# Kernel optimization log

Measured on AMD Instinct MI355X. Metric: run time of the kernel, lower is better.

The kernel has to match this reference:

```python
import jax, jax.numpy as jnp
import numpy as np

B, D, E, H = 8192, 2048, 8, 128

def setup_inputs() -> dict:
    key = jax.random.key(0)
    ks = jax.random.split(key, 9)
    s_d = 1.0 / np.sqrt(D)
    s_h = 1.0 / np.sqrt(H)
    return {
        "x": jax.random.normal(ks[0], (B, D), dtype=jnp.float32),
        "gate_w": jax.random.normal(ks[1], (D, E), dtype=jnp.float32) * s_d,
        "gate_b": jnp.zeros((E,), dtype=jnp.float32),
        "W1": jax.random.normal(ks[2], (E, D, H), dtype=jnp.float32) * s_d,
        "b1": jnp.zeros((E, H), dtype=jnp.float32),
        "W2": jax.random.normal(ks[3], (E, H, H), dtype=jnp.float32) * s_h,
        "b2": jnp.zeros((E, H), dtype=jnp.float32),
        "W3": jax.random.normal(ks[4], (E, H, D), dtype=jnp.float32) * s_h,
        "b3": jnp.zeros((E, D), dtype=jnp.float32),
    }

def reference(x, gate_w, gate_b, W1, b1, W2, b2, W3, b3):
    # Adaptive gate: softmax over experts
    gates = jax.nn.softmax(x @ gate_w + gate_b, axis=1)          # [B, E]
    # All experts as one batched (grouped) GEMM over the expert axis.
    h1 = jax.nn.silu(jnp.einsum('bd,edh->ebh', x, W1) + b1[:, None, :])   # [E, B, H]
    h2 = jax.nn.silu(jnp.einsum('ebh,ehk->ebk', h1, W2) + b2[:, None, :]) # [E, B, H]
    y = jnp.einsum('ebh,ehd->ebd', h2, W3) + b3[:, None, :]               # [E, B, D]
    # Gate-weighted sum over experts (fused reduction, no [B,E,D] stack kept)
    out = jnp.einsum('be,ebd->bd', gates, y)                     # [B, D]
    return out
```

## Files before the change

### kernel.cpp

```cpp
#include <hip/hip_runtime.h>


typedef __attribute__((ext_vector_type(8))) short short8;
typedef __attribute__((ext_vector_type(4))) float f32x4;

#define B_SZ 8192
#define D_SZ 2048
#define E_SZ 8
#define H_SZ 128
#define TILE_ELEMS 8192

__device__ __forceinline__ short f2bf(float f) {
  unsigned u = __builtin_bit_cast(unsigned, f);
  unsigned r = (u + 0x7fffu + ((u >> 16) & 1u)) >> 16;
  return (short)r;
}

__device__ __forceinline__ float silu_f(float v) {
  return v / (1.f + __expf(-v));
}

__device__ __forceinline__ void gload_lds16(const void* g, void* l) {
  __builtin_amdgcn_global_load_lds(
      (const __attribute__((address_space(1))) void*)g,
      (__attribute__((address_space(3))) void*)l,
      16, 0, 0);
}

template<int NKT>
__device__ __forceinline__ void gemm_core(const short* __restrict__ Ab,
                                          const short* __restrict__ Bb,
                                          short* lds, f32x4 acc[4][4])
{
  const int tid  = threadIdx.x;
  const int lane = tid & 63;
  const int wid  = tid >> 6;
  const int wr = wid >> 1, wc = wid & 1;
  const int lm = lane & 15, lk = lane >> 4;
  const int wbase = tid & ~63;
  short* As = lds;
  short* Bs = lds + 2 * TILE_ELEMS;

  #pragma unroll
  for (int q = 0; q < 4; ++q) {
    gload_lds16(Ab + (q*256 + tid)*8, As + (q*256 + wbase)*8);
    gload_lds16(Bb + (q*256 + tid)*8, Bs + (q*256 + wbase)*8);
  }
  __syncthreads();

  for (int kt = 0; kt < NKT; ++kt) {
    const int cur = kt & 1;
    if (kt + 1 < NKT) {
      const short* ga = Ab + (size_t)(kt+1)*TILE_ELEMS;
      const short* gb = Bb + (size_t)(kt+1)*TILE_ELEMS;
      short* la = As + (cur^1)*TILE_ELEMS;
      short* lb = Bs + (cur^1)*TILE_ELEMS;
      #pragma unroll
      for (int q = 0; q < 4; ++q) {
        gload_lds16(ga + (q*256 + tid)*8, la + (q*256 + wbase)*8);
        gload_lds16(gb + (q*256 + tid)*8, lb + (q*256 + wbase)*8);
      }
    }
    const short* Ac = As + cur*TILE_ELEMS;
    const short* Bc = Bs + cur*TILE_ELEMS;
    #pragma unroll
    for (int ks = 0; ks < 2; ++ks) {
      short8 av[4], bv[4];
      #pragma unroll
      for (int f = 0; f < 4; ++f)
        av[f] = *(const short8*)(Ac + (ks*4 + lk)*1024 + (wr*64 + f*16 + lm)*8);
      #pragma unroll
      for (int f = 0; f < 4; ++f)
        bv[f] = *(const short8*)(Bc + (ks*4 + lk)*1024 + (wc*64 + f*16 + lm)*8);
      #pragma unroll
      for (int i = 0; i < 4; ++i)
        #pragma unroll
        for (int j = 0; j < 4; ++j)
          acc[i][j] = __builtin_amdgcn_mfma_f32_16x16x32_bf16(av[i], bv[j], acc[i][j], 0, 0, 0);
    }
    __syncthreads();
  }
}

__global__ __launch_bounds__(256)
void k_convert(const float* __restrict__ x,  const float* __restrict__ W1,
               const float* __restrict__ W2, const float* __restrict__ W3,
               short* __restrict__ xf, short* __restrict__ w1f,
               short* __restrict__ w2f, short* __restrict__ w3f)
{
  const int gi = blockIdx.x * 256 + threadIdx.x;
  if (gi < 2097152) {
    const int t = gi >> 10, r = gi & 1023;
    const int bt = t >> 5, kt = t & 31;
    const int kg = r >> 7, p = r & 127;
    const float* src = x + (size_t)(bt*128 + p)*2048 + kt*64 + kg*8;
    const float4 v0 = *(const float4*)src;
    const float4 v1 = *(const float4*)(src + 4);
    short8 o;
    o[0]=f2bf(v0.x); o[1]=f2bf(v0.y); o[2]=f2bf(v0.z); o[3]=f2bf(v0.w);
    o[4]=f2bf(v1.x); o[5]=f2bf(v1.y); o[6]=f2bf(v1.z); o[7]=f2bf(v1.w);
    *(short8*)(xf + (size_t)gi*8) = o;
  } else if (gi < 2097152 + 262144) {
    const int g = gi - 2097152;
    const int t = g >> 10, r = g & 1023;
    const int e = t >> 5, kt = t & 31;
    const int kg = r >> 7, p = r & 127;
    const int k0 = kt*64 + kg*8;
    short8 o;
    #pragma unroll
    for (int j = 0; j < 8; ++j)
      o[j] = f2bf(W1[(size_t)e*262144 + (size_t)(k0 + j)*128 + p]);
    *(short8*)(w1f + (size_t)g*8) = o;
  } else if (gi < 2097152 + 262144 + 16384) {
    const int g = gi - (2097152 + 262144);
    const int t = g >> 10, r = g & 1023;
    const int e = t >> 1, kt = t & 1;
    const int kg = r >> 7, p = r & 127;
    const int k0 = kt*64 + kg*8;
    short8 o;
    #pragma unroll
    for (int j = 0; j < 8; ++j)
      o[j] = f2bf(W2[(size_t)e*16384 + (size_t)(k0 + j)*128 + p]);
    *(short8*)(w2f + (size_t)g*8) = o;
  } else if (gi < 2637824) {
    const int g = gi - 2375680;
    const int t = g >> 10, r = g & 1023;
    const int nt = t >> 4, kt = t & 15;
    const int kg = r >> 7, p = r & 127;
    const int k0 = kt*64 + kg*8;
    short8 o;
    #pragma unroll
    for (int j = 0; j < 8; ++j) {
      const int k = k0 + j;
      o[j] = f2bf(W3[(size_t)(k >> 7)*262144 + (size_t)(k & 127)*2048 + nt*128 + p]);
    }
    *(short8*)(w3f + (size_t)g*8) = o;
  }
}

__global__ __launch_bounds__(256)
void k_gate(const float* __restrict__ x, const float* __restrict__ gw,
            const float* __restrict__ gb, float* __restrict__ gates)
{
  const int wid = threadIdx.x >> 6, lane = threadIdx.x & 63;
  const int row = blockIdx.x * 4 + wid;
  const float* xr = x + (size_t)row * 2048;
  float acc[8] = {0.f,0.f,0.f,0.f,0.f,0.f,0.f,0.f};
  for (int it = 0; it < 32; ++it) {
    const int k = it*64 + lane;
    const float xv = xr[k];
    const float4 g0 = *(const float4*)(gw + (size_t)k*8);
    const float4 g1 = *(const float4*)(gw + (size_t)k*8 + 4);
    acc[0] += xv*g0.x; acc[1] += xv*g0.y; acc[2] += xv*g0.z; acc[3] += xv*g0.w;
    acc[4] += xv*g1.x; acc[5] += xv*g1.y; acc[6] += xv*g1.z; acc[7] += xv*g1.w;
  }
  #pragma unroll
  for (int e = 0; e < 8; ++e) {
    #pragma unroll
    for (int d = 1; d < 64; d <<= 1)
      acc[e] += __shfl_xor(acc[e], d, 64);
  }
  if (lane == 0) {
    float lg[8], mx = -1e30f;
    #pragma unroll
    for (int e = 0; e < 8; ++e) { lg[e] = acc[e] + gb[e]; mx = fmaxf(mx, lg[e]); }
    float s = 0.f;
    #pragma unroll
    for (int e = 0; e < 8; ++e) { lg[e] = __expf(lg[e] - mx); s += lg[e]; }
    const float inv = 1.f / s;
    #pragma unroll
    for (int e = 0; e < 8; ++e) gates[(size_t)row*8 + e] = lg[e] * inv;
  }
}

__global__ __launch_bounds__(256, 2)
void k_gemm1(const short* __restrict__ xf, const short* __restrict__ w1f,
             const float* __restrict__ b1, short* __restrict__ h1f)
{
  __shared__ short lds[4 * TILE_ELEMS];
  const int bt = blockIdx.x, e = blockIdx.y;
  f32x4 acc[4][4] = {};
  gemm_core<32>(xf + (size_t)bt*32*TILE_ELEMS, w1f + (size_t)e*32*TILE_ELEMS, lds, acc);

  const int tid = threadIdx.x, lane = tid & 63, wid = tid >> 6;
  const int wr = wid >> 1, wc = wid & 1, lm = lane & 15;
  float bv[4];
  #pragma unroll
  for (int fn = 0; fn < 4; ++fn) bv[fn] = b1[e*H_SZ + wc*64 + fn*16 + lm];
  #pragma unroll
  for (int fm = 0; fm < 4; ++fm)
  #pragma unroll
  for (int i = 0; i < 4; ++i) {
    const int m = wr*64 + fm*16 + (lane>>4)*4 + i;
    #pragma unroll
    for (int fn = 0; fn < 4; ++fn) {
      const int n = wc*64 + fn*16 + lm;
      float v = silu_f(acc[fm][fn][i] + bv[fn]);
      lds[(n>>6)*TILE_ELEMS + ((n>>3)&7)*1024 + m*8 + (n&7)] = f2bf(v);
    }
  }
  __syncthreads();
  short* gout = h1f + (size_t)e*1048576 + (size_t)bt*16384;
  #pragma unroll
  for (int q = 0; q < 8; ++q) {
    const int li = q*256 + tid;
    *(short8*)(gout + li*8) = *(const short8*)(lds + li*8);
  }
}

__global__ __launch_bounds__(256, 2)
void k_gemm2(const short* __restrict__ h1f, const short* __restrict__ w2f,
             const float* __restrict__ b2, const float* __restrict__ gates,
             short* __restrict__ h2gf)
{
  __shared__ short lds[4 * TILE_ELEMS];
  const int bt = blockIdx.x, e = blockIdx.y;
  f32x4 acc[4][4] = {};
  gemm_core<2>(h1f + (size_t)e*1048576 + (size_t)bt*16384,
               w2f + (size_t)e*2*TILE_ELEMS, lds, acc);

  const int tid = threadIdx.x, lane = tid & 63, wid = tid >> 6;
  const int wr = wid >> 1, wc = wid & 1, lm = lane & 15;
  float bv[4];
  #pragma unroll
  for (int fn = 0; fn < 4; ++fn) bv[fn] = b2[e*H_SZ + wc*64 + fn*16 + lm];
  #pragma unroll
  for (int fm = 0; fm < 4; ++fm)
  #pragma unroll
  for (int i = 0; i < 4; ++i) {
    const int m = wr*64 + fm*16 + (lane>>4)*4 + i;
    const float g = gates[(size_t)(bt*128 + m)*8 + e];
    #pragma unroll
    for (int fn = 0; fn < 4; ++fn) {
      const int n = wc*64 + fn*16 + lm;
      float v = silu_f(acc[fm][fn][i] + bv[fn]) * g;
      lds[(n>>6)*TILE_ELEMS + ((n>>3)&7)*1024 + m*8 + (n&7)] = f2bf(v);
    }
  }
  __syncthreads();
  short* gout = h2gf + (size_t)bt*16384*8 + (size_t)e*16384;
  #pragma unroll
  for (int q = 0; q < 8; ++q) {
    const int li = q*256 + tid;
    *(short8*)(gout + li*8) = *(const short8*)(lds + li*8);
  }
}

__global__ __launch_bounds__(256, 2)
void k_gemm3(const short* __restrict__ h2gf, const short* __restrict__ w3f,
             const float* __restrict__ b3, const float* __restrict__ gates,
             float* __restrict__ out)
{
  __shared__ short lds[4 * TILE_ELEMS];
  const int bt = blockIdx.x, nt = blockIdx.y;
  f32x4 acc[4][4] = {};
  gemm_core<16>(h2gf + (size_t)bt*16*TILE_ELEMS, w3f + (size_t)nt*16*TILE_ELEMS, lds, acc);

  const int tid = threadIdx.x, lane = tid & 63, wid = tid >> 6;
  const int wr = wid >> 1, wc = wid & 1, lm = lane & 15;
  float b3c[4][8];
  #pragma unroll
  for (int fn = 0; fn < 4; ++fn) {
    const int n = nt*128 + wc*64 + fn*16 + lm;
    #pragma unroll
    for (int e = 0; e < 8; ++e) b3c[fn][e] = b3[(size_t)e*D_SZ + n];
  }
  #pragma unroll
  for (int fm = 0; fm < 4; ++fm)
  #pragma unroll
  for (int i = 0; i < 4; ++i) {
    const int m = bt*128 + wr*64 + fm*16 + (lane>>4)*4 + i;
    const float4 ga = *(const float4*)(gates + (size_t)m*8);
    const float4 gbv = *(const float4*)(gates + (size_t)m*8 + 4);
    #pragma unroll
    for (int fn = 0; fn < 4; ++fn) {
      const int n = nt*128 + wc*64 + fn*16 + lm;
      const float bias = ga.x*b3c[fn][0] + ga.y*b3c[fn][1] + ga.z*b3c[fn][2] + ga.w*b3c[fn][3]
                       + gbv.x*b3c[fn][4] + gbv.y*b3c[fn][5] + gbv.z*b3c[fn][6] + gbv.w*b3c[fn][7];
      out[(size_t)m*D_SZ + n] = acc[fm][fn][i] + bias;
    }
  }
}

extern "C" void kernel_launch(void* const* d_in, const int* in_sizes, int n_in,
                              void* d_out, int out_size, void* d_ws, size_t ws_size,
                              hipStream_t stream)
{
  (void)in_sizes; (void)n_in; (void)out_size; (void)ws_size;
  const float* x  = (const float*)d_in[0];
  const float* gw = (const float*)d_in[1];
  const float* gb = (const float*)d_in[2];
  const float* W1 = (const float*)d_in[3];
  const float* b1 = (const float*)d_in[4];
  const float* W2 = (const float*)d_in[5];
  const float* b2 = (const float*)d_in[6];
  const float* W3 = (const float*)d_in[7];
  const float* b3 = (const float*)d_in[8];
  float* out = (float*)d_out;

  char* ws = (char*)d_ws;
  short* xf    = (short*)ws;  ws += (size_t)B_SZ*D_SZ*2;
  short* w1f   = (short*)ws;  ws += (size_t)E_SZ*D_SZ*H_SZ*2;
  short* w2f   = (short*)ws;  ws += (size_t)E_SZ*H_SZ*H_SZ*2;
  short* w3f   = (short*)ws;  ws += (size_t)E_SZ*H_SZ*D_SZ*2;
  float* gates = (float*)ws;  ws += (size_t)B_SZ*E_SZ*4;
  short* h1f   = (short*)ws;  ws += (size_t)E_SZ*B_SZ*H_SZ*2;
  short* h2gf  = (short*)ws;  ws += (size_t)B_SZ*E_SZ*H_SZ*2;

  k_convert<<<dim3(10304), dim3(256), 0, stream>>>(x, W1, W2, W3, xf, w1f, w2f, w3f);
  k_gate   <<<dim3(2048),  dim3(256), 0, stream>>>(x, gw, gb, gates);
  k_gemm1  <<<dim3(64, 8), dim3(256), 0, stream>>>(xf, w1f, b1, h1f);
  k_gemm2  <<<dim3(64, 8), dim3(256), 0, stream>>>(h1f, w2f, b2, gates, h2gf);
  k_gemm3  <<<dim3(64, 16), dim3(256), 0, stream>>>(h2gf, w3f, b3, gates, out);
}
```

Baseline: 151.2 us.

## Use 8-wave 256x128 tiles with double-buffered half-K pipelined GEMM core

Adds a new GEMM core for gemm1 and gemm3 that uses 512-thread blocks computing 256x128 output tiles, with double-buffered LDS staging split into K halves. Global-to-LDS loads for upcoming stages overlap MFMA work, using explicit vmcnt waits, barriers and raised MFMA priority. The larger tile improves B-operand reuse and halves the grid. The risks are higher LDS usage and lower occupancy, and the hand-placed waits and barriers are fragile to get right.

```diff
diff --git a/kernel.cpp b/kernel.cpp
--- a/kernel.cpp
+++ b/kernel.cpp
@@ -10,6 +10,11 @@
 #define H_SZ 128
 #define TILE_ELEMS 8192
 
+#define VMCNT(n) asm volatile("s_waitcnt vmcnt(" #n ")" ::: "memory")
+#define LGKM0()  asm volatile("s_waitcnt lgkmcnt(0)" ::: "memory")
+#define SB0()    __builtin_amdgcn_sched_barrier(0)
+#define BAR()    __builtin_amdgcn_s_barrier()
+
 __device__ __forceinline__ short f2bf(float f) {
   unsigned u = __builtin_bit_cast(unsigned, f);
   unsigned r = (u + 0x7fffu + ((u >> 16) & 1u)) >> 16;
@@ -25,6 +30,94 @@
       (const __attribute__((address_space(1))) void*)g,
       (__attribute__((address_space(3))) void*)l,
       16, 0, 0);
+}
+
+template<int NKT>
+__device__ __forceinline__ void core8(const short* __restrict__ Ab,
+                                      const short* __restrict__ Bb,
+                                      short* lds, f32x4 acc[4][4])
+{
+  const int tid  = threadIdx.x;
+  const int lane = tid & 63;
+  const int wid  = tid >> 6;
+  const int wm = wid >> 1, wn = wid & 1;
+  const int rt = wm >> 1, rh = wm & 1;
+  const int lm = lane & 15, lk = lane >> 4;
+  const int wlds = (tid & ~63) * 8;
+
+  auto STAGE = [&](int b, int tau, int kh) {
+    const int boff = b * 24576;
+    gload_lds16(Ab + (size_t)(0*NKT + tau)*8192 + kh*4096 + tid*8,
+                lds + boff + 0*8192 + kh*4096 + wlds);
+    gload_lds16(Ab + (size_t)(1*NKT + tau)*8192 + kh*4096 + tid*8,
+                lds + boff + 1*8192 + kh*4096 + wlds);
+    gload_lds16(Bb + (size_t)tau*8192 + kh*4096 + tid*8,
+                lds + boff + 16384 + kh*4096 + wlds);
+  };
+  auto READ_A = [&](int ks, int cur, short8 av[4]) {
+    const short* Ac = lds + cur*24576 + rt*8192 + (ks*4+lk)*1024 + (rh*64 + lm)*8;
+    #pragma unroll
+    for (int f = 0; f < 4; ++f) av[f] = *(const short8*)(Ac + f*128);
+  };
+  auto READ_B = [&](int ks, int cur, short8 bv[4]) {
+    const short* Bc = lds + cur*24576 + 16384 + (ks*4+lk)*1024 + (wn*64 + lm)*8;
+    #pragma unroll
+    for (int f = 0; f < 4; ++f) bv[f] = *(const short8*)(Bc + f*128);
+  };
+  auto MFMA16 = [&](short8 av[4], short8 bv[4]) {
+    __builtin_amdgcn_s_setprio(1);
+    #pragma unroll
+    for (int i = 0; i < 4; ++i)
+      #pragma unroll
+      for (int j = 0; j < 4; ++j)
+        acc[i][j] = __builtin_amdgcn_mfma_f32_16x16x32_bf16(av[i], bv[j], acc[i][j], 0, 0, 0);
+    __builtin_amdgcn_s_setprio(0);
+  };
+
+  STAGE(0, 0, 0);
+  STAGE(0, 0, 1);
+  STAGE(1, 1, 0);
+  VMCNT(6); BAR();
+
+  for (int t = 0; t < NKT - 2; ++t) {
+    const int cur = t & 1;
+    short8 av[4], bv[4];
+    READ_A(0, cur, av); READ_B(0, cur, bv);
+    STAGE(cur ^ 1, t + 1, 1);
+    BAR(); LGKM0(); SB0();
+    MFMA16(av, bv);
+    SB0(); VMCNT(6); BAR();
+    READ_A(1, cur, av); READ_B(1, cur, bv);
+    STAGE(cur, t + 2, 0);
+    BAR(); LGKM0(); SB0();
+    MFMA16(av, bv);
+    SB0(); VMCNT(6); BAR();
+  }
+  {
+    const int cur = (NKT - 2) & 1;
+    short8 av[4], bv[4];
+    READ_A(0, cur, av); READ_B(0, cur, bv);
+    STAGE(cur ^ 1, NKT - 1, 1);
+    BAR(); LGKM0(); SB0();
+    MFMA16(av, bv);
+    SB0(); VMCNT(6); BAR();
+    READ_A(1, cur, av); READ_B(1, cur, bv);
+    BAR(); LGKM0(); SB0();
+    MFMA16(av, bv);
+    SB0(); VMCNT(3); BAR();
+  }
+  {
+    const int cur = (NKT - 1) & 1;
+    short8 av[4], bv[4];
+    READ_A(0, cur, av); READ_B(0, cur, bv);
+    BAR(); LGKM0(); SB0();
+    MFMA16(av, bv);
+    SB0(); VMCNT(0); BAR();
+    READ_A(1, cur, av); READ_B(1, cur, bv);
+    BAR(); LGKM0(); SB0();
+    MFMA16(av, bv);
+    SB0();
+  }
 }
 
 template<int NKT>
@@ -173,38 +266,41 @@
   }
 }
 
-__global__ __launch_bounds__(256, 2)
+__global__ __launch_bounds__(512, 2)
 void k_gemm1(const short* __restrict__ xf, const short* __restrict__ w1f,
              const float* __restrict__ b1, short* __restrict__ h1f)
 {
-  __shared__ short lds[4 * TILE_ELEMS];
+  __shared__ short lds[49152];
   const int bt = blockIdx.x, e = blockIdx.y;
   f32x4 acc[4][4] = {};
-  gemm_core<32>(xf + (size_t)bt*32*TILE_ELEMS, w1f + (size_t)e*32*TILE_ELEMS, lds, acc);
-
+  core8<32>(xf + (size_t)(bt*2)*32*8192, w1f + (size_t)e*32*8192, lds, acc);
+
+  __syncthreads();
   const int tid = threadIdx.x, lane = tid & 63, wid = tid >> 6;
-  const int wr = wid >> 1, wc = wid & 1, lm = lane & 15;
+  const int wm = wid >> 1, wn = wid & 1, lm = lane & 15, lr = lane >> 4;
   float bv[4];
   #pragma unroll
-  for (int fn = 0; fn < 4; ++fn) bv[fn] = b1[e*H_SZ + wc*64 + fn*16 + lm];
+  for (int fn = 0; fn < 4; ++fn) bv[fn] = b1[e*H_SZ + wn*64 + fn*16 + lm];
   #pragma unroll
   for (int fm = 0; fm < 4; ++fm)
   #pragma unroll
   for (int i = 0; i < 4; ++i) {
-    const int m = wr*64 + fm*16 + (lane>>4)*4 + i;
+    const int m = wm*64 + fm*16 + lr*4 + i;
     #pragma unroll
     for (int fn = 0; fn < 4; ++fn) {
-      const int n = wc*64 + fn*16 + lm;
+      const int n = wn*64 + fn*16 + lm;
       float v = silu_f(acc[fm][fn][i] + bv[fn]);
-      lds[(n>>6)*TILE_ELEMS + ((n>>3)&7)*1024 + m*8 + (n&7)] = f2bf(v);
+      lds[(m>>7)*16384 + (n>>6)*8192 + ((n>>3)&7)*1024 + (m&127)*8 + (n&7)] = f2bf(v);
     }
   }
   __syncthreads();
-  short* gout = h1f + (size_t)e*1048576 + (size_t)bt*16384;
   #pragma unroll
   for (int q = 0; q < 8; ++q) {
-    const int li = q*256 + tid;
-    *(short8*)(gout + li*8) = *(const short8*)(lds + li*8);
+    const int li = q*4096 + tid*8;
+    const int ti = li >> 13, o = li & 8191;
+    const int rt_o = ti >> 1, kt_o = ti & 1;
+    short* dst = h1f + ((size_t)(e*64 + bt*2 + rt_o)*2 + kt_o)*8192 + o;
+    *(short8*)dst = *(const short8*)(lds + li);
   }
 }
 
@@ -246,22 +342,22 @@
   }
 }
 
-__global__ __launch_bounds__(256, 2)
+__global__ __launch_bounds__(512, 2)
 void k_gemm3(const short* __restrict__ h2gf, const short* __restrict__ w3f,
              const float* __restrict__ b3, const float* __restrict__ gates,
              float* __restrict__ out)
 {
-  __shared__ short lds[4 * TILE_ELEMS];
+  __shared__ short lds[49152];
   const int bt = blockIdx.x, nt = blockIdx.y;
   f32x4 acc[4][4] = {};
-  gemm_core<16>(h2gf + (size_t)bt*16*TILE_ELEMS, w3f + (size_t)nt*16*TILE_ELEMS, lds, acc);
+  core8<16>(h2gf + (size_t)(bt*2)*16*8192, w3f + (size_t)nt*16*8192, lds, acc);
 
   const int tid = threadIdx.x, lane = tid & 63, wid = tid >> 6;
-  const int wr = wid >> 1, wc = wid & 1, lm = lane & 15;
+  const int wm = wid >> 1, wn = wid & 1, lm = lane & 15, lr = lane >> 4;
   float b3c[4][8];
   #pragma unroll
   for (int fn = 0; fn < 4; ++fn) {
-    const int n = nt*128 + wc*64 + fn*16 + lm;
+    const int n = nt*128 + wn*64 + fn*16 + lm;
     #pragma unroll
     for (int e = 0; e < 8; ++e) b3c[fn][e] = b3[(size_t)e*D_SZ + n];
   }
@@ -269,12 +365,12 @@
   for (int fm = 0; fm < 4; ++fm)
   #pragma unroll
   for (int i = 0; i < 4; ++i) {
-    const int m = bt*128 + wr*64 + fm*16 + (lane>>4)*4 + i;
-    const float4 ga = *(const float4*)(gates + (size_t)m*8);
+    const int m = bt*256 + wm*64 + fm*16 + lr*4 + i;
+    const float4 ga  = *(const float4*)(gates + (size_t)m*8);
     const float4 gbv = *(const float4*)(gates + (size_t)m*8 + 4);
     #pragma unroll
     for (int fn = 0; fn < 4; ++fn) {
-      const int n = nt*128 + wc*64 + fn*16 + lm;
+      const int n = nt*128 + wn*64 + fn*16 + lm;
       const float bias = ga.x*b3c[fn][0] + ga.y*b3c[fn][1] + ga.z*b3c[fn][2] + ga.w*b3c[fn][3]
                        + gbv.x*b3c[fn][4] + gbv.y*b3c[fn][5] + gbv.z*b3c[fn][6] + gbv.w*b3c[fn][7];
       out[(size_t)m*D_SZ + n] = acc[fm][fn][i] + bias;
@@ -309,7 +405,7 @@
 
   k_convert<<<dim3(10304), dim3(256), 0, stream>>>(x, W1, W2, W3, xf, w1f, w2f, w3f);
   k_gate   <<<dim3(2048),  dim3(256), 0, stream>>>(x, gw, gb, gates);
-  k_gemm1  <<<dim3(64, 8), dim3(256), 0, stream>>>(xf, w1f, b1, h1f);
-  k_gemm2  <<<dim3(64, 8), dim3(256), 0, stream>>>(h1f, w2f, b2, gates, h2gf);
-  k_gemm3  <<<dim3(64, 16), dim3(256), 0, stream>>>(h2gf, w3f, b3, gates, out);
-}
+  k_gemm1  <<<dim3(32, 8),  dim3(512), 0, stream>>>(xf, w1f, b1, h1f);
+  k_gemm2  <<<dim3(64, 8),  dim3(256), 0, stream>>>(h1f, w2f, b2, gates, h2gf);
+  k_gemm3  <<<dim3(32, 16), dim3(512), 0, stream>>>(h2gf, w3f, b3, gates, out);
+}
```

Measured after the change: 154.1 us. About the same (+2.0%).

## Fuse expert GEMM1 and GEMM2, enlarge tiles, add XCD-aware block mapping

Applied to the files above, without the earlier changes.

Merges the first two expert GEMMs into one kernel, so the SiLU(h1) tile stays in LDS and is fed straight into the W2 GEMM. This removes the h1 round trip through global memory and one launch. The kernels move to 512-thread blocks with larger tiles (128x256 for GEMM1, 256x256 for GEMM3) and a half-K-step pipeline that uses explicit vmcnt waits. Blocks are remapped so that neighbouring batch tiles land on the same XCD. The larger tiles mean more register pressure and only 256 workgroups per launch, which may limit occupancy and overlap.

```diff
diff --git a/kernel.cpp b/kernel.cpp
--- a/kernel.cpp
+++ b/kernel.cpp
@@ -8,7 +8,9 @@
 #define D_SZ 2048
 #define E_SZ 8
 #define H_SZ 128
-#define TILE_ELEMS 8192
+
+#define VMCNT(n) asm volatile("s_waitcnt vmcnt(" #n ")" ::: "memory")
+#define BAR()    __builtin_amdgcn_s_barrier()
 
 __device__ __forceinline__ short f2bf(float f) {
   unsigned u = __builtin_bit_cast(unsigned, f);
@@ -25,61 +27,6 @@
       (const __attribute__((address_space(1))) void*)g,
       (__attribute__((address_space(3))) void*)l,
       16, 0, 0);
-}
-
-template<int NKT>
-__device__ __forceinline__ void gemm_core(const short* __restrict__ Ab,
-                                          const short* __restrict__ Bb,
-                                          short* lds, f32x4 acc[4][4])
-{
-  const int tid  = threadIdx.x;
-  const int lane = tid & 63;
-  const int wid  = tid >> 6;
-  const int wr = wid >> 1, wc = wid & 1;
-  const int lm = lane & 15, lk = lane >> 4;
-  const int wbase = tid & ~63;
-  short* As = lds;
-  short* Bs = lds + 2 * TILE_ELEMS;
-
-  #pragma unroll
-  for (int q = 0; q < 4; ++q) {
-    gload_lds16(Ab + (q*256 + tid)*8, As + (q*256 + wbase)*8);
-    gload_lds16(Bb + (q*256 + tid)*8, Bs + (q*256 + wbase)*8);
-  }
-  __syncthreads();
-
-  for (int kt = 0; kt < NKT; ++kt) {
-    const int cur = kt & 1;
-    if (kt + 1 < NKT) {
-      const short* ga = Ab + (size_t)(kt+1)*TILE_ELEMS;
-      const short* gb = Bb + (size_t)(kt+1)*TILE_ELEMS;
-      short* la = As + (cur^1)*TILE_ELEMS;
-      short* lb = Bs + (cur^1)*TILE_ELEMS;
-      #pragma unroll
-      for (int q = 0; q < 4; ++q) {
-        gload_lds16(ga + (q*256 + tid)*8, la + (q*256 + wbase)*8);
-        gload_lds16(gb + (q*256 + tid)*8, lb + (q*256 + wbase)*8);
-      }
-    }
-    const short* Ac = As + cur*TILE_ELEMS;
-    const short* Bc = Bs + cur*TILE_ELEMS;
-    #pragma unroll
-    for (int ks = 0; ks < 2; ++ks) {
-      short8 av[4], bv[4];
-      #pragma unroll
-      for (int f = 0; f < 4; ++f)
-        av[f] = *(const short8*)(Ac + (ks*4 + lk)*1024 + (wr*64 + f*16 + lm)*8);
-      #pragma unroll
-      for (int f = 0; f < 4; ++f)
-        bv[f] = *(const short8*)(Bc + (ks*4 + lk)*1024 + (wc*64 + f*16 + lm)*8);
-      #pragma unroll
-      for (int i = 0; i < 4; ++i)
-        #pragma unroll
-        for (int j = 0; j < 4; ++j)
-          acc[i][j] = __builtin_amdgcn_mfma_f32_16x16x32_bf16(av[i], bv[j], acc[i][j], 0, 0, 0);
-    }
-    __syncthreads();
-  }
 }
 
 __global__ __launch_bounds__(256)
@@ -173,108 +120,214 @@
   }
 }
 
-__global__ __launch_bounds__(256, 2)
-void k_gemm1(const short* __restrict__ xf, const short* __restrict__ w1f,
-             const float* __restrict__ b1, short* __restrict__ h1f)
-{
-  __shared__ short lds[4 * TILE_ELEMS];
-  const int bt = blockIdx.x, e = blockIdx.y;
+__global__ __launch_bounds__(512, 2)
+void k_gemm12(const short* __restrict__ xf, const short* __restrict__ w1f,
+              const short* __restrict__ w2f,
+              const float* __restrict__ b1, const float* __restrict__ b2,
+              const float* __restrict__ gates, short* __restrict__ h2gf)
+{
+  __shared__ short lds[65536];
+  const int wg = blockIdx.x;
+  const int xcd = wg & 7, idx = wg >> 3;
+  const int bt = xcd*8 + (idx >> 2);
+  const int nt = idx & 3;
+
+  const int tid  = threadIdx.x;
+  const int lane = tid & 63;
+  const int wid  = tid >> 6;
+  const int wm = wid >> 2, wn = wid & 3;
+  const int lm = lane & 15, lk = lane >> 4, lr = lane >> 4;
+  const int wlds = (tid & ~63) * 8;
+
+  const short* Ab  = xf + (size_t)bt*32*8192;
+  const short* Bb0 = w1f + (size_t)(2*nt)*32*8192;
+  const short* Bb1 = w1f + (size_t)(2*nt+1)*32*8192;
+
   f32x4 acc[4][4] = {};
-  gemm_core<32>(xf + (size_t)bt*32*TILE_ELEMS, w1f + (size_t)e*32*TILE_ELEMS, lds, acc);
-
-  const int tid = threadIdx.x, lane = tid & 63, wid = tid >> 6;
-  const int wr = wid >> 1, wc = wid & 1, lm = lane & 15;
-  float bv[4];
-  #pragma unroll
-  for (int fn = 0; fn < 4; ++fn) bv[fn] = b1[e*H_SZ + wc*64 + fn*16 + lm];
+
+  auto STAGE = [&](int n2) {
+    const int tau = n2 >> 1, ks = n2 & 1, b = tau & 1;
+    gload_lds16(Ab  + (size_t)tau*8192 + ks*4096 + tid*8,
+                lds + b*24576 + ks*4096 + wlds);
+    gload_lds16(Bb0 + (size_t)tau*8192 + ks*4096 + tid*8,
+                lds + b*24576 + 8192 + ks*4096 + wlds);
+    gload_lds16(Bb1 + (size_t)tau*8192 + ks*4096 + tid*8,
+                lds + b*24576 + 16384 + ks*4096 + wlds);
+  };
+
+  STAGE(0); STAGE(1);
+  VMCNT(3); BAR();
+
+  for (int n = 0; n < 64; ++n) {
+    const int tau = n >> 1, ks = n & 1, b = tau & 1;
+    if (n + 2 < 64) STAGE(n + 2);
+    short8 av[4], bv[4];
+    #pragma unroll
+    for (int f = 0; f < 4; ++f)
+      av[f] = *(const short8*)(lds + b*24576 + (ks*4+lk)*1024 + (wm*64 + f*16 + lm)*8);
+    #pragma unroll
+    for (int f = 0; f < 4; ++f)
+      bv[f] = *(const short8*)(lds + b*24576 + 8192 + (wn>>1)*8192 + (ks*4+lk)*1024
+                               + ((wn&1)*64 + f*16 + lm)*8);
+    #pragma unroll
+    for (int i = 0; i < 4; ++i)
+      #pragma unroll
+      for (int j = 0; j < 4; ++j)
+        acc[i][j] = __builtin_amdgcn_mfma_f32_16x16x32_bf16(av[i], bv[j], acc[i][j], 0, 0, 0);
+    if (n + 2 < 64)      { VMCNT(3); BAR(); }
+    else if (n + 1 < 64) { VMCNT(0); BAR(); }
+  }
+  BAR();
+
+  #pragma unroll
+  for (int q = 0; q < 8; ++q)
+    gload_lds16(w2f + (size_t)nt*32768 + q*4096 + tid*8, lds + 32768 + q*4096 + wlds);
+
+  float b1v[4];
+  #pragma unroll
+  for (int fn = 0; fn < 4; ++fn) b1v[fn] = b1[nt*256 + wn*64 + fn*16 + lm];
   #pragma unroll
   for (int fm = 0; fm < 4; ++fm)
   #pragma unroll
   for (int i = 0; i < 4; ++i) {
-    const int m = wr*64 + fm*16 + (lane>>4)*4 + i;
+    const int m = wm*64 + fm*16 + lr*4 + i;
     #pragma unroll
     for (int fn = 0; fn < 4; ++fn) {
-      const int n = wc*64 + fn*16 + lm;
-      float v = silu_f(acc[fm][fn][i] + bv[fn]);
-      lds[(n>>6)*TILE_ELEMS + ((n>>3)&7)*1024 + m*8 + (n&7)] = f2bf(v);
-    }
-  }
-  __syncthreads();
-  short* gout = h1f + (size_t)e*1048576 + (size_t)bt*16384;
-  #pragma unroll
-  for (int q = 0; q < 8; ++q) {
-    const int li = q*256 + tid;
-    *(short8*)(gout + li*8) = *(const short8*)(lds + li*8);
-  }
-}
-
-__global__ __launch_bounds__(256, 2)
-void k_gemm2(const short* __restrict__ h1f, const short* __restrict__ w2f,
-             const float* __restrict__ b2, const float* __restrict__ gates,
-             short* __restrict__ h2gf)
-{
-  __shared__ short lds[4 * TILE_ELEMS];
-  const int bt = blockIdx.x, e = blockIdx.y;
-  f32x4 acc[4][4] = {};
-  gemm_core<2>(h1f + (size_t)e*1048576 + (size_t)bt*16384,
-               w2f + (size_t)e*2*TILE_ELEMS, lds, acc);
-
-  const int tid = threadIdx.x, lane = tid & 63, wid = tid >> 6;
-  const int wr = wid >> 1, wc = wid & 1, lm = lane & 15;
-  float bv[4];
-  #pragma unroll
-  for (int fn = 0; fn < 4; ++fn) bv[fn] = b2[e*H_SZ + wc*64 + fn*16 + lm];
-  #pragma unroll
-  for (int fm = 0; fm < 4; ++fm)
-  #pragma unroll
-  for (int i = 0; i < 4; ++i) {
-    const int m = wr*64 + fm*16 + (lane>>4)*4 + i;
-    const float g = gates[(size_t)(bt*128 + m)*8 + e];
-    #pragma unroll
-    for (int fn = 0; fn < 4; ++fn) {
-      const int n = wc*64 + fn*16 + lm;
-      float v = silu_f(acc[fm][fn][i] + bv[fn]) * g;
-      lds[(n>>6)*TILE_ELEMS + ((n>>3)&7)*1024 + m*8 + (n&7)] = f2bf(v);
-    }
-  }
-  __syncthreads();
-  short* gout = h2gf + (size_t)bt*16384*8 + (size_t)e*16384;
-  #pragma unroll
-  for (int q = 0; q < 8; ++q) {
-    const int li = q*256 + tid;
-    *(short8*)(gout + li*8) = *(const short8*)(lds + li*8);
-  }
-}
-
-__global__ __launch_bounds__(256, 2)
+      const int n = wn*64 + fn*16 + lm;
+      const float v = silu_f(acc[fm][fn][i] + b1v[fn]);
+      lds[(n>>7)*16384 + ((n>>6)&1)*8192 + ((n>>3)&7)*1024 + m*8 + (n&7)] = f2bf(v);
+    }
+  }
+  VMCNT(0); BAR();
+
+  const int wm2 = wid >> 2, wn2 = wid & 3;
+  #pragma unroll
+  for (int eh = 0; eh < 2; ++eh) {
+    f32x4 acc2[4][2] = {};
+    #pragma unroll
+    for (int kt2 = 0; kt2 < 2; ++kt2)
+    #pragma unroll
+    for (int ks = 0; ks < 2; ++ks) {
+      short8 a2[4], b2v[2];
+      #pragma unroll
+      for (int f = 0; f < 4; ++f)
+        a2[f] = *(const short8*)(lds + eh*16384 + kt2*8192 + (ks*4+lk)*1024
+                                 + (wm2*64 + f*16 + lm)*8);
+      #pragma unroll
+      for (int f = 0; f < 2; ++f)
+        b2v[f] = *(const short8*)(lds + 32768 + eh*16384 + kt2*8192 + (ks*4+lk)*1024
+                                  + (wn2*32 + f*16 + lm)*8);
+      #pragma unroll
+      for (int i = 0; i < 4; ++i)
+        #pragma unroll
+        for (int j = 0; j < 2; ++j)
+          acc2[i][j] = __builtin_amdgcn_mfma_f32_16x16x32_bf16(a2[i], b2v[j], acc2[i][j], 0, 0, 0);
+    }
+    BAR();
+
+    const int e = 2*nt + eh;
+    #pragma unroll
+    for (int fm = 0; fm < 4; ++fm)
+    #pragma unroll
+    for (int i = 0; i < 4; ++i) {
+      const int m = wm2*64 + fm*16 + lr*4 + i;
+      const float g = gates[(size_t)(bt*128 + m)*8 + e];
+      #pragma unroll
+      for (int fn = 0; fn < 2; ++fn) {
+        const int h = wn2*32 + fn*16 + lm;
+        const float v = silu_f(acc2[fm][fn][i] + b2[e*128 + h]) * g;
+        lds[32768 + ((h>>6)&1)*8192 + ((h>>3)&7)*1024 + m*8 + (h&7)] = f2bf(v);
+      }
+    }
+    BAR();
+    #pragma unroll
+    for (int q = 0; q < 4; ++q) {
+      const int li = q*4096 + tid*8;
+      const int t2 = li >> 13, o = li & 8191;
+      *(short8*)(h2gf + ((size_t)bt*16 + 2*e + t2)*8192 + o) =
+          *(const short8*)(lds + 32768 + li);
+    }
+    if (eh == 0) BAR();
+  }
+}
+
+__global__ __launch_bounds__(512, 2)
 void k_gemm3(const short* __restrict__ h2gf, const short* __restrict__ w3f,
              const float* __restrict__ b3, const float* __restrict__ gates,
              float* __restrict__ out)
 {
-  __shared__ short lds[4 * TILE_ELEMS];
-  const int bt = blockIdx.x, nt = blockIdx.y;
-  f32x4 acc[4][4] = {};
-  gemm_core<16>(h2gf + (size_t)bt*16*TILE_ELEMS, w3f + (size_t)nt*16*TILE_ELEMS, lds, acc);
-
-  const int tid = threadIdx.x, lane = tid & 63, wid = tid >> 6;
-  const int wr = wid >> 1, wc = wid & 1, lm = lane & 15;
+  __shared__ short lds[65536];
+  const int wg = blockIdx.x;
+  const int xcd = wg & 7, idx = wg >> 3;
+  const int bt = xcd*4 + (idx & 3);
+  const int nt = idx >> 2;
+
+  const int tid  = threadIdx.x;
+  const int lane = tid & 63;
+  const int wid  = tid >> 6;
+  const int wm = wid >> 2, wn = wid & 3;
+  const int lm = lane & 15, lk = lane >> 4, lr = lane >> 4;
+  const int wlds = (tid & ~63) * 8;
+
+  const short* A0 = h2gf + (size_t)(bt*2)*16*8192;
+  const short* A1 = h2gf + (size_t)(bt*2+1)*16*8192;
+  const short* B0 = w3f + (size_t)(2*nt)*16*8192;
+  const short* B1 = w3f + (size_t)(2*nt+1)*16*8192;
+
+  f32x4 acc[8][4] = {};
+
+  auto STAGE = [&](int n2) {
+    const int tau = n2 >> 1, ks = n2 & 1, b = tau & 1;
+    gload_lds16(A0 + (size_t)tau*8192 + ks*4096 + tid*8,
+                lds + b*32768 + ks*4096 + wlds);
+    gload_lds16(A1 + (size_t)tau*8192 + ks*4096 + tid*8,
+                lds + b*32768 + 8192 + ks*4096 + wlds);
+    gload_lds16(B0 + (size_t)tau*8192 + ks*4096 + tid*8,
+                lds + b*32768 + 16384 + ks*4096 + wlds);
+    gload_lds16(B1 + (size_t)tau*8192 + ks*4096 + tid*8,
+                lds + b*32768 + 24576 + ks*4096 + wlds);
+  };
+
+  STAGE(0); STAGE(1);
+  VMCNT(4); BAR();
+
+  for (int n = 0; n < 32; ++n) {
+    const int tau = n >> 1, ks = n & 1, b = tau & 1;
+    if (n + 2 < 32) STAGE(n + 2);
+    short8 av[8], bv[4];
+    #pragma unroll
+    for (int f = 0; f < 8; ++f)
+      av[f] = *(const short8*)(lds + b*32768 + wm*8192 + (ks*4+lk)*1024 + (f*16 + lm)*8);
+    #pragma unroll
+    for (int f = 0; f < 4; ++f)
+      bv[f] = *(const short8*)(lds + b*32768 + 16384 + (wn>>1)*8192 + (ks*4+lk)*1024
+                               + ((wn&1)*64 + f*16 + lm)*8);
+    #pragma unroll
+    for (int i = 0; i < 8; ++i)
+      #pragma unroll
+      for (int j = 0; j < 4; ++j)
+        acc[i][j] = __builtin_amdgcn_mfma_f32_16x16x32_bf16(av[i], bv[j], acc[i][j], 0, 0, 0);
+    if (n + 2 < 32)      { VMCNT(4); BAR(); }
+    else if (n + 1 < 32) { VMCNT(0); BAR(); }
+  }
+
   float b3c[4][8];
   #pragma unroll
   for (int fn = 0; fn < 4; ++fn) {
-    const int n = nt*128 + wc*64 + fn*16 + lm;
+    const int n = nt*256 + wn*64 + fn*16 + lm;
     #pragma unroll
     for (int e = 0; e < 8; ++e) b3c[fn][e] = b3[(size_t)e*D_SZ + n];
   }
   #pragma unroll
-  for (int fm = 0; fm < 4; ++fm)
+  for (int fm = 0; fm < 8; ++fm)
   #pragma unroll
   for (int i = 0; i < 4; ++i) {
-    const int m = bt*128 + wr*64 + fm*16 + (lane>>4)*4 + i;
-    const float4 ga = *(const float4*)(gates + (size_t)m*8);
+    const int m = bt*256 + wm*128 + fm*16 + lr*4 + i;
+    const float4 ga  = *(const float4*)(gates + (size_t)m*8);
     const float4 gbv = *(const float4*)(gates + (size_t)m*8 + 4);
     #pragma unroll
     for (int fn = 0; fn < 4; ++fn) {
-      const int n = nt*128 + wc*64 + fn*16 + lm;
+      const int n = nt*256 + wn*64 + fn*16 + lm;
       const float bias = ga.x*b3c[fn][0] + ga.y*b3c[fn][1] + ga.z*b3c[fn][2] + ga.w*b3c[fn][3]
                        + gbv.x*b3c[fn][4] + gbv.y*b3c[fn][5] + gbv.z*b3c[fn][6] + gbv.w*b3c[fn][7];
       out[(size_t)m*D_SZ + n] = acc[fm][fn][i] + bias;
@@ -304,12 +357,10 @@
   short* w2f   = (short*)ws;  ws += (size_t)E_SZ*H_SZ*H_SZ*2;
   short* w3f   = (short*)ws;  ws += (size_t)E_SZ*H_SZ*D_SZ*2;
   float* gates = (float*)ws;  ws += (size_t)B_SZ*E_SZ*4;
-  short* h1f   = (short*)ws;  ws += (size_t)E_SZ*B_SZ*H_SZ*2;
   short* h2gf  = (short*)ws;  ws += (size_t)B_SZ*E_SZ*H_SZ*2;
 
   k_convert<<<dim3(10304), dim3(256), 0, stream>>>(x, W1, W2, W3, xf, w1f, w2f, w3f);
   k_gate   <<<dim3(2048),  dim3(256), 0, stream>>>(x, gw, gb, gates);
-  k_gemm1  <<<dim3(64, 8), dim3(256), 0, stream>>>(xf, w1f, b1, h1f);
-  k_gemm2  <<<dim3(64, 8), dim3(256), 0, stream>>>(h1f, w2f, b2, gates, h2gf);
-  k_gemm3  <<<dim3(64, 16), dim3(256), 0, stream>>>(h2gf, w3f, b3, gates, out);
-}
+  k_gemm12 <<<dim3(256), dim3(512), 0, stream>>>(xf, w1f, w2f, b1, b2, gates, h2gf);
+  k_gemm3  <<<dim3(256), dim3(512), 0, stream>>>(h2gf, w3f, b3, gates, out);
+}
```

Measured after the change: 141.1 us. -6.7%, faster.
